# Kernel tuning notes

Hardware: AMD Instinct MI355X
Metric: run time of the kernel (lower is better)

The kernel has to match this reference:

```python
import jax, jax.numpy as jnp
import numpy as np

N_NODES = 100000
N_EDGES = 600000
F_IN, HID, CLS = 128, 128, 16


def sage_conv(x, src, dst, W_l, b_l, W_r, n_nodes):
    # mean aggregation of neighbor features: message x[src] scattered to dst
    msg = x[src]                                              # [E, F]
    agg = jax.ops.segment_sum(msg, dst, num_segments=n_nodes)  # [N, F]
    deg = jax.ops.segment_sum(jnp.ones((src.shape[0],), x.dtype), dst, num_segments=n_nodes)
    agg = agg / jnp.maximum(deg, 1.0)[:, None]
    # PyG SAGEConv: lin_l(agg) (with bias) + lin_r(x_root) (no bias)
    return agg @ W_l + b_l + x @ W_r


def setup_inputs() -> dict:
    key = jax.random.key(0)
    ks = jax.random.split(key, 6)
    x = jax.random.normal(ks[0], (N_NODES, F_IN), jnp.float32)
    edge_index = jax.random.randint(ks[1], (2, N_EDGES), 0, N_NODES, dtype=jnp.int64)
    s1 = 1.0 / np.sqrt(F_IN)
    s2 = 1.0 / np.sqrt(HID)
    return {
        "x": x,
        "edge_index": edge_index,
        "W1_l": jax.random.normal(ks[2], (F_IN, HID), jnp.float32) * s1,
        "b1": jnp.zeros((HID,), jnp.float32),
        "W1_r": jax.random.normal(ks[3], (F_IN, HID), jnp.float32) * s1,
        "W2_l": jax.random.normal(ks[4], (HID, CLS), jnp.float32) * s2,
        "b2": jnp.zeros((CLS,), jnp.float32),
        "W2_r": jax.random.normal(ks[5], (HID, CLS), jnp.float32) * s2,
    }


def reference(x, edge_index, W1_l, b1, W1_r, W2_l, b2, W2_r):
    n = x.shape[0]
    src, dst = edge_index[0], edge_index[1]
    h = sage_conv(x, src, dst, W1_l, b1, W1_r, n)
    h = jax.nn.relu(h)
    # F.dropout(training=self.training): identity in eval mode
    out = sage_conv(h, src, dst, W2_l, b2, W2_r, n)
    return jax.nn.log_softmax(out, axis=1)
```

## Files before the change

### kernel.cpp

```cpp
#include <hip/hip_runtime.h>
#include <cstdint>

#define N_NODES 100000
#define N_PAD 100096
#define N_EDGES 600000
#define F 128
#define CLS 16
#define CAP 64

typedef short bf16x8 __attribute__((ext_vector_type(8)));
typedef float f32x4 __attribute__((ext_vector_type(4)));

__device__ inline float bf2f(unsigned int lo16) { return __uint_as_float(lo16 << 16); }
__device__ inline unsigned short f2b(float f) {
    unsigned int u = __float_as_uint(f);
    return (unsigned short)((u + 0x7fffu + ((u >> 16) & 1u)) >> 16);
}

__global__ __launch_bounds__(256) void init_k(int* __restrict__ deg,
                                              const float* __restrict__ x,
                                              unsigned short* __restrict__ xb,
                                              const float* __restrict__ W1l,
                                              const float* __restrict__ W1r,
                                              const float* __restrict__ W2l,
                                              const float* __restrict__ W2r,
                                              unsigned short* __restrict__ w1t,
                                              unsigned short* __restrict__ w2t) {
    int b = blockIdx.x;
    if (b < 98) {
        int i = b * 1024 + threadIdx.x * 4;
#pragma unroll
        for (int k = 0; k < 4; k++)
            if (i + k < N_NODES) deg[i + k] = 0;
    } else if (b < 12598) {
        int i = (b - 98) * 256 + threadIdx.x;
        if (i < N_NODES * F / 4) {
            float4 v = ((const float4*)x)[i];
            ushort4 o;
            o.x = f2b(v.x); o.y = f2b(v.y); o.z = f2b(v.z); o.w = f2b(v.w);
            ((ushort4*)xb)[i] = o;
        }
    } else if (b < 12726) {
        int idx = (b - 12598) * 256 + threadIdx.x;
        int n = idx >> 8, k = idx & 255;
        float v = (k < F) ? W1l[k * F + n] : W1r[(k - F) * F + n];
        w1t[idx] = f2b(v);
    } else {
        int idx = (b - 12726) * 256 + threadIdx.x;
        if (idx < 32 * F) {
            int n = idx >> 7, k = idx & 127;
            float v = (n < CLS) ? W2l[k * CLS + n] : W2r[k * CLS + (n - CLS)];
            w2t[idx] = f2b(v);
        }
    }
}

__global__ void fill_k(const int* __restrict__ src, const int* __restrict__ dst,
                       int* __restrict__ deg, int* __restrict__ bucket) {
    int e = blockIdx.x * blockDim.x + threadIdx.x;
    if (e < N_EDGES) {
        int d = dst[e];
        int slot = atomicAdd(&deg[d], 1);
        if (slot < CAP) bucket[d * CAP + slot] = src[e];
    }
}

__global__ __launch_bounds__(256) void agg_b_k(const unsigned short* __restrict__ feat,
                                               const int* __restrict__ deg,
                                               const int* __restrict__ bucket,
                                               unsigned short* __restrict__ outagg) {
    int node = blockIdx.x * 4 + (threadIdx.x >> 6);
    int lane = threadIdx.x & 63;
    int r = lane >> 4;
    int f8 = (lane & 15) * 8;
    const int* bk = bucket + node * CAP;

    int d_raw = deg[node];
    int nb0r = bk[r];
    int nb1r = bk[4 + r];
    int nb0 = min(max(nb0r, 0), N_NODES - 1);
    int nb1 = min(max(nb1r, 0), N_NODES - 1);
    uint4 v0 = *(const uint4*)(feat + (size_t)nb0 * F + f8);
    uint4 v1 = *(const uint4*)(feat + (size_t)nb1 * F + f8);

    int d = min(d_raw, CAP);
    float acc[8] = {0.f, 0.f, 0.f, 0.f, 0.f, 0.f, 0.f, 0.f};
    if (r < d) {
        acc[0] += bf2f(v0.x & 0xffffu); acc[1] += bf2f(v0.x >> 16);
        acc[2] += bf2f(v0.y & 0xffffu); acc[3] += bf2f(v0.y >> 16);
        acc[4] += bf2f(v0.z & 0xffffu); acc[5] += bf2f(v0.z >> 16);
        acc[6] += bf2f(v0.w & 0xffffu); acc[7] += bf2f(v0.w >> 16);
    }
    if (4 + r < d) {
        acc[0] += bf2f(v1.x & 0xffffu); acc[1] += bf2f(v1.x >> 16);
        acc[2] += bf2f(v1.y & 0xffffu); acc[3] += bf2f(v1.y >> 16);
        acc[4] += bf2f(v1.z & 0xffffu); acc[5] += bf2f(v1.z >> 16);
        acc[6] += bf2f(v1.w & 0xffffu); acc[7] += bf2f(v1.w >> 16);
    }
    for (int j = 8; j < d; j += 8) {
        int i0 = j + r, i1 = j + 4 + r;
        bool ok0 = i0 < d, ok1 = i1 < d;
        int m0 = bk[ok0 ? i0 : 0];
        int m1 = bk[ok1 ? i1 : 0];
        uint4 w0 = *(const uint4*)(feat + (size_t)m0 * F + f8);
        uint4 w1 = *(const uint4*)(feat + (size_t)m1 * F + f8);
        if (ok0) {
            acc[0] += bf2f(w0.x & 0xffffu); acc[1] += bf2f(w0.x >> 16);
            acc[2] += bf2f(w0.y & 0xffffu); acc[3] += bf2f(w0.y >> 16);
            acc[4] += bf2f(w0.z & 0xffffu); acc[5] += bf2f(w0.z >> 16);
            acc[6] += bf2f(w0.w & 0xffffu); acc[7] += bf2f(w0.w >> 16);
        }
        if (ok1) {
            acc[0] += bf2f(w1.x & 0xffffu); acc[1] += bf2f(w1.x >> 16);
            acc[2] += bf2f(w1.y & 0xffffu); acc[3] += bf2f(w1.y >> 16);
            acc[4] += bf2f(w1.z & 0xffffu); acc[5] += bf2f(w1.z >> 16);
            acc[6] += bf2f(w1.w & 0xffffu); acc[7] += bf2f(w1.w >> 16);
        }
    }
#pragma unroll
    for (int i = 0; i < 8; i++) {
        acc[i] += __shfl_xor(acc[i], 16);
        acc[i] += __shfl_xor(acc[i], 32);
    }
    if (r == 0) {
        float inv = 1.0f / fmaxf((float)d, 1.0f);
        uint4 o;
        o.x = (unsigned int)f2b(acc[0] * inv) | ((unsigned int)f2b(acc[1] * inv) << 16);
        o.y = (unsigned int)f2b(acc[2] * inv) | ((unsigned int)f2b(acc[3] * inv) << 16);
        o.z = (unsigned int)f2b(acc[4] * inv) | ((unsigned int)f2b(acc[5] * inv) << 16);
        o.w = (unsigned int)f2b(acc[6] * inv) | ((unsigned int)f2b(acc[7] * inv) << 16);
        *(uint4*)(outagg + (size_t)node * F + f8) = o;
    }
}

__global__ __launch_bounds__(256) void gemm_fused(const unsigned short* __restrict__ Ab,
                                                  const unsigned short* __restrict__ Xb,
                                                  const unsigned short* __restrict__ Wt,
                                                  const float* __restrict__ bias,
                                                  const unsigned short* __restrict__ Wt2,
                                                  float* __restrict__ trL,
                                                  float* __restrict__ trR) {
    __shared__ unsigned short sw[64 * 512];
    __shared__ unsigned short sw2[8 * 512];
    int tid = threadIdx.x;
#pragma unroll
    for (int i = 0; i < 16; i++) {
        int idx8 = i * 256 + tid;
        uint4 v = ((const uint4*)Wt)[idx8];
        int n = idx8 >> 5;
        int k0 = (idx8 & 31) * 8;
        int ct = n >> 4, m = n & 15;
        int half = k0 >> 7, ks = (k0 >> 5) & 3, quad = (k0 >> 3) & 3;
        int frag = ct * 8 + ks * 2 + half;
        int lane = quad * 16 + m;
        *(uint4*)&sw[frag * 512 + lane * 8] = v;
    }
#pragma unroll
    for (int i = 0; i < 2; i++) {
        int idx8 = i * 256 + tid;
        uint4 v = ((const uint4*)Wt2)[idx8];
        int n = idx8 >> 4;
        int k0 = (idx8 & 15) * 8;
        int tile = n >> 4, m = n & 15;
        int ks = k0 >> 5, quad = (k0 >> 3) & 3;
        int frag = tile * 4 + ks;
        int lane = quad * 16 + m;
        *(uint4*)&sw2[frag * 512 + lane * 8] = v;
    }
    __syncthreads();

    int wave = tid >> 6, lane = tid & 63;
    int row0 = blockIdx.x * 128 + wave * 32;
    int m = lane & 15, quad = lane >> 4;
    int koff = quad * 8;

    const unsigned short* pa0 = Ab + (size_t)(row0 + m) * F + koff;
    const unsigned short* pa1 = pa0 + 16 * F;
    const unsigned short* px0 = Xb + (size_t)(row0 + m) * F + koff;
    const unsigned short* px1 = px0 + 16 * F;
    const unsigned short* swl = sw + lane * 8;

    f32x4 acc0[8], acc1[8];
#pragma unroll
    for (int ct = 0; ct < 8; ct++) { acc0[ct] = (f32x4){0,0,0,0}; acc1[ct] = (f32x4){0,0,0,0}; }

#pragma unroll
    for (int ks = 0; ks < 4; ks++) {
        bf16x8 a0 = *(const bf16x8*)(const void*)(pa0 + ks * 32);
        bf16x8 a1 = *(const bf16x8*)(const void*)(pa1 + ks * 32);
        bf16x8 x0 = *(const bf16x8*)(const void*)(px0 + ks * 32);
        bf16x8 x1 = *(const bf16x8*)(const void*)(px1 + ks * 32);
#pragma unroll
        for (int ct = 0; ct < 8; ct++) {
            bf16x8 bl = *(const bf16x8*)(const void*)(swl + (ct * 8 + ks * 2 + 0) * 512);
            bf16x8 br = *(const bf16x8*)(const void*)(swl + (ct * 8 + ks * 2 + 1) * 512);
            acc0[ct] = __builtin_amdgcn_mfma_f32_16x16x32_bf16(a0, bl, acc0[ct], 0, 0, 0);
            acc1[ct] = __builtin_amdgcn_mfma_f32_16x16x32_bf16(a1, bl, acc1[ct], 0, 0, 0);
            acc0[ct] = __builtin_amdgcn_mfma_f32_16x16x32_bf16(x0, br, acc0[ct], 0, 0, 0);
            acc1[ct] = __builtin_amdgcn_mfma_f32_16x16x32_bf16(x1, br, acc1[ct], 0, 0, 0);
        }
    }
    __syncthreads();

    int lr0 = wave * 32 + quad * 4;
#pragma unroll
    for (int ct = 0; ct < 8; ct++) {
        int n = ct * 16 + m;
        float bv = bias[n];
#pragma unroll
        for (int r = 0; r < 4; r++) {
            sw[(lr0 + r) * 132 + n]      = f2b(fmaxf(acc0[ct][r] + bv, 0.f));
            sw[(lr0 + 16 + r) * 132 + n] = f2b(fmaxf(acc1[ct][r] + bv, 0.f));
        }
    }
    __syncthreads();

    const unsigned short* hl0 = sw + (wave * 32 + m) * 132 + koff;
    const unsigned short* hl1 = sw + (wave * 32 + 16 + m) * 132 + koff;
    const unsigned short* sw2l = sw2 + lane * 8;

    f32x4 al0 = (f32x4){0,0,0,0}, al1 = (f32x4){0,0,0,0};
    f32x4 ar0 = (f32x4){0,0,0,0}, ar1 = (f32x4){0,0,0,0};
#pragma unroll
    for (int ks = 0; ks < 4; ks++) {
        bf16x8 h0 = *(const bf16x8*)(const void*)(hl0 + ks * 32);
        bf16x8 h1 = *(const bf16x8*)(const void*)(hl1 + ks * 32);
        bf16x8 wl = *(const bf16x8*)(const void*)(sw2l + (0 * 4 + ks) * 512);
        bf16x8 wr = *(const bf16x8*)(const void*)(sw2l + (1 * 4 + ks) * 512);
        al0 = __builtin_amdgcn_mfma_f32_16x16x32_bf16(h0, wl, al0, 0, 0, 0);
        al1 = __builtin_amdgcn_mfma_f32_16x16x32_bf16(h1, wl, al1, 0, 0, 0);
        ar0 = __builtin_amdgcn_mfma_f32_16x16x32_bf16(h0, wr, ar0, 0, 0, 0);
        ar1 = __builtin_amdgcn_mfma_f32_16x16x32_bf16(h1, wr, ar1, 0, 0, 0);
    }
    int r0 = row0 + quad * 4;
#pragma unroll
    for (int r = 0; r < 4; r++) {
        trL[(size_t)(r0 + r) * CLS + m]      = al0[r];
        trL[(size_t)(r0 + 16 + r) * CLS + m] = al1[r];
        trR[(size_t)(r0 + r) * CLS + m]      = ar0[r];
        trR[(size_t)(r0 + 16 + r) * CLS + m] = ar1[r];
    }
}

__global__ __launch_bounds__(256) void agg2sm_k(const float* __restrict__ trL,
                                                const float* __restrict__ trR,
                                                const int* __restrict__ deg,
                                                const int* __restrict__ bucket,
                                                const float* __restrict__ b2,
                                                float* __restrict__ out) {
    int node = blockIdx.x * 4 + (threadIdx.x >> 6);
    int lane = threadIdx.x & 63;
    int r = lane >> 2;
    int cq = (lane & 3) * 4;
    const int* bk = bucket + node * CAP;

    int d_raw = deg[node];
    int nbr = bk[r];
    int nb = min(max(nbr, 0), N_NODES - 1);
    float4 v = *(const float4*)(trL + (size_t)nb * CLS + cq);
    float4 selfR = *(const float4*)(trR + (size_t)node * CLS + cq);

    int d = min(d_raw, CAP);
    float4 acc = {0.f, 0.f, 0.f, 0.f};
    if (r < d) { acc.x += v.x; acc.y += v.y; acc.z += v.z; acc.w += v.w; }
    for (int j = 16; j < d; j += 16) {
        int idx = j + r;
        bool valid = idx < d;
        int m2 = bk[valid ? idx : 0];
        float4 w = *(const float4*)(trL + (size_t)m2 * CLS + cq);
        if (valid) { acc.x += w.x; acc.y += w.y; acc.z += w.z; acc.w += w.w; }
    }
#pragma unroll
    for (int off = 4; off <= 32; off <<= 1) {
        acc.x += __shfl_xor(acc.x, off);
        acc.y += __shfl_xor(acc.y, off);
        acc.z += __shfl_xor(acc.z, off);
        acc.w += __shfl_xor(acc.w, off);
    }
    float inv = 1.0f / fmaxf((float)d, 1.0f);
    float4 bb = *(const float4*)(b2 + cq);
    float vx = acc.x * inv + selfR.x + bb.x;
    float vy = acc.y * inv + selfR.y + bb.y;
    float vz = acc.z * inv + selfR.z + bb.z;
    float vw = acc.w * inv + selfR.w + bb.w;
    float mx = fmaxf(fmaxf(vx, vy), fmaxf(vz, vw));
    mx = fmaxf(mx, __shfl_xor(mx, 1));
    mx = fmaxf(mx, __shfl_xor(mx, 2));
    float sm = __expf(vx - mx) + __expf(vy - mx) + __expf(vz - mx) + __expf(vw - mx);
    sm += __shfl_xor(sm, 1);
    sm += __shfl_xor(sm, 2);
    float lg = __logf(sm);
    if (r == 0) {
        float4 o = {vx - mx - lg, vy - mx - lg, vz - mx - lg, vw - mx - lg};
        *(float4*)(out + (size_t)node * CLS + cq) = o;
    }
}


extern "C" void kernel_launch(void* const* d_in, const int* in_sizes, int n_in,
                              void* d_out, int out_size, void* d_ws, size_t ws_size,
                              hipStream_t stream) {
    const float* x   = (const float*)d_in[0];
    const int*   ei  = (const int*)d_in[1];
    const float* W1l = (const float*)d_in[2];
    const float* b1  = (const float*)d_in[3];
    const float* W1r = (const float*)d_in[4];
    const float* W2l = (const float*)d_in[5];
    const float* b2  = (const float*)d_in[6];
    const float* W2r = (const float*)d_in[7];
    float* out = (float*)d_out;

    const int* src = ei;
    const int* dst = ei + N_EDGES;

    char* ws = (char*)d_ws;
    size_t off = 0;
    auto alloc = [&](size_t bytes) { char* p = ws + off; off += (bytes + 127) / 128 * 128; return p; };
    int* deg    = (int*)alloc((size_t)N_NODES * 4);
    int* bucket = (int*)alloc((size_t)N_NODES * CAP * 4);
    unsigned short* xb   = (unsigned short*)alloc((size_t)N_PAD * F * 2);
    unsigned short* aggb = (unsigned short*)alloc((size_t)N_PAD * F * 2);
    float*          trL  = (float*)alloc((size_t)N_PAD * CLS * 4);
    float*          trR  = (float*)alloc((size_t)N_PAD * CLS * 4);
    unsigned short* w1t  = (unsigned short*)alloc((size_t)F * 256 * 2);
    unsigned short* w2t  = (unsigned short*)alloc((size_t)32 * F * 2);

    init_k<<<12743, 256, 0, stream>>>(deg, x, xb, W1l, W1r, W2l, W2r, w1t, w2t);
    fill_k<<<(N_EDGES + 255) / 256, 256, 0, stream>>>(src, dst, deg, bucket);
    agg_b_k<<<N_NODES / 4, 256, 0, stream>>>(xb, deg, bucket, aggb);
    gemm_fused<<<N_PAD / 128, 256, 0, stream>>>(aggb, xb, w1t, b1, w2t, trL, trR);
    agg2sm_k<<<N_NODES / 4, 256, 0, stream>>>(trL, trR, deg, bucket, b2, out);
}
```

Measured before the change: 225.1 us.

## Pre-swizzle weights into MFMA fragment order and read B operands from global

The init kernel now writes the transposed bf16 weights directly in MFMA fragment-major order. The fused GEMM therefore drops its per-block staging of the weights into shared memory and one barrier, and loads B fragments straight from global memory, where they are expected to stay cache resident. Shared memory shrinks to the hidden-activation buffer only, which may raise occupancy. The cost is that every B fragment load now goes to global/L2 with higher latency instead of LDS.

```diff
diff --git a/kernel.cpp b/kernel.cpp
--- a/kernel.cpp
+++ b/kernel.cpp
@@ -44,13 +44,17 @@
         int idx = (b - 12598) * 256 + threadIdx.x;
         int n = idx >> 8, k = idx & 255;
         float v = (k < F) ? W1l[k * F + n] : W1r[(k - F) * F + n];
-        w1t[idx] = f2b(v);
+        int ct = n >> 4, m = n & 15;
+        int half = k >> 7, ks = (k >> 5) & 3, quad = (k >> 3) & 3, j = k & 7;
+        w1t[(ct * 8 + ks * 2 + half) * 512 + (quad * 16 + m) * 8 + j] = f2b(v);
     } else {
         int idx = (b - 12726) * 256 + threadIdx.x;
         if (idx < 32 * F) {
             int n = idx >> 7, k = idx & 127;
             float v = (n < CLS) ? W2l[k * CLS + n] : W2r[k * CLS + (n - CLS)];
-            w2t[idx] = f2b(v);
+            int tile = n >> 4, m = n & 15;
+            int ks = (k >> 5) & 3, quad = (k >> 3) & 3, j = k & 7;
+            w2t[(tile * 4 + ks) * 512 + (quad * 16 + m) * 8 + j] = f2b(v);
         }
     }
 }
@@ -140,35 +144,8 @@
                                                   const unsigned short* __restrict__ Wt2,
                                                   float* __restrict__ trL,
                                                   float* __restrict__ trR) {
-    __shared__ unsigned short sw[64 * 512];
-    __shared__ unsigned short sw2[8 * 512];
+    __shared__ unsigned short sh[128 * 132];
     int tid = threadIdx.x;
-#pragma unroll
-    for (int i = 0; i < 16; i++) {
-        int idx8 = i * 256 + tid;
-        uint4 v = ((const uint4*)Wt)[idx8];
-        int n = idx8 >> 5;
-        int k0 = (idx8 & 31) * 8;
-        int ct = n >> 4, m = n & 15;
-        int half = k0 >> 7, ks = (k0 >> 5) & 3, quad = (k0 >> 3) & 3;
-        int frag = ct * 8 + ks * 2 + half;
-        int lane = quad * 16 + m;
-        *(uint4*)&sw[frag * 512 + lane * 8] = v;
-    }
-#pragma unroll
-    for (int i = 0; i < 2; i++) {
-        int idx8 = i * 256 + tid;
-        uint4 v = ((const uint4*)Wt2)[idx8];
-        int n = idx8 >> 4;
-        int k0 = (idx8 & 15) * 8;
-        int tile = n >> 4, m = n & 15;
-        int ks = k0 >> 5, quad = (k0 >> 3) & 3;
-        int frag = tile * 4 + ks;
-        int lane = quad * 16 + m;
-        *(uint4*)&sw2[frag * 512 + lane * 8] = v;
-    }
-    __syncthreads();
-
     int wave = tid >> 6, lane = tid & 63;
     int row0 = blockIdx.x * 128 + wave * 32;
     int m = lane & 15, quad = lane >> 4;
@@ -178,7 +155,7 @@
     const unsigned short* pa1 = pa0 + 16 * F;
     const unsigned short* px0 = Xb + (size_t)(row0 + m) * F + koff;
     const unsigned short* px1 = px0 + 16 * F;
-    const unsigned short* swl = sw + lane * 8;
+    const unsigned short* pw = Wt + lane * 8;
 
     f32x4 acc0[8], acc1[8];
 #pragma unroll
@@ -192,15 +169,14 @@
         bf16x8 x1 = *(const bf16x8*)(const void*)(px1 + ks * 32);
 #pragma unroll
         for (int ct = 0; ct < 8; ct++) {
-            bf16x8 bl = *(const bf16x8*)(const void*)(swl + (ct * 8 + ks * 2 + 0) * 512);
-            bf16x8 br = *(const bf16x8*)(const void*)(swl + (ct * 8 + ks * 2 + 1) * 512);
+            bf16x8 bl = *(const bf16x8*)(const void*)(pw + (ct * 8 + ks * 2 + 0) * 512);
+            bf16x8 br = *(const bf16x8*)(const void*)(pw + (ct * 8 + ks * 2 + 1) * 512);
             acc0[ct] = __builtin_amdgcn_mfma_f32_16x16x32_bf16(a0, bl, acc0[ct], 0, 0, 0);
             acc1[ct] = __builtin_amdgcn_mfma_f32_16x16x32_bf16(a1, bl, acc1[ct], 0, 0, 0);
             acc0[ct] = __builtin_amdgcn_mfma_f32_16x16x32_bf16(x0, br, acc0[ct], 0, 0, 0);
             acc1[ct] = __builtin_amdgcn_mfma_f32_16x16x32_bf16(x1, br, acc1[ct], 0, 0, 0);
         }
     }
-    __syncthreads();
 
     int lr0 = wave * 32 + quad * 4;
 #pragma unroll
@@ -209,15 +185,15 @@
         float bv = bias[n];
 #pragma unroll
         for (int r = 0; r < 4; r++) {
-            sw[(lr0 + r) * 132 + n]      = f2b(fmaxf(acc0[ct][r] + bv, 0.f));
-            sw[(lr0 + 16 + r) * 132 + n] = f2b(fmaxf(acc1[ct][r] + bv, 0.f));
+            sh[(lr0 + r) * 132 + n]      = f2b(fmaxf(acc0[ct][r] + bv, 0.f));
+            sh[(lr0 + 16 + r) * 132 + n] = f2b(fmaxf(acc1[ct][r] + bv, 0.f));
         }
     }
     __syncthreads();
 
-    const unsigned short* hl0 = sw + (wave * 32 + m) * 132 + koff;
-    const unsigned short* hl1 = sw + (wave * 32 + 16 + m) * 132 + koff;
-    const unsigned short* sw2l = sw2 + lane * 8;
+    const unsigned short* hl0 = sh + (wave * 32 + m) * 132 + koff;
+    const unsigned short* hl1 = sh + (wave * 32 + 16 + m) * 132 + koff;
+    const unsigned short* pw2 = Wt2 + lane * 8;
 
     f32x4 al0 = (f32x4){0,0,0,0}, al1 = (f32x4){0,0,0,0};
     f32x4 ar0 = (f32x4){0,0,0,0}, ar1 = (f32x4){0,0,0,0};
@@ -225,8 +201,8 @@
     for (int ks = 0; ks < 4; ks++) {
         bf16x8 h0 = *(const bf16x8*)(const void*)(hl0 + ks * 32);
         bf16x8 h1 = *(const bf16x8*)(const void*)(hl1 + ks * 32);
-        bf16x8 wl = *(const bf16x8*)(const void*)(sw2l + (0 * 4 + ks) * 512);
-        bf16x8 wr = *(const bf16x8*)(const void*)(sw2l + (1 * 4 + ks) * 512);
+        bf16x8 wl = *(const bf16x8*)(const void*)(pw2 + (0 * 4 + ks) * 512);
+        bf16x8 wr = *(const bf16x8*)(const void*)(pw2 + (1 * 4 + ks) * 512);
         al0 = __builtin_amdgcn_mfma_f32_16x16x32_bf16(h0, wl, al0, 0, 0, 0);
         al1 = __builtin_amdgcn_mfma_f32_16x16x32_bf16(h1, wl, al1, 0, 0, 0);
         ar0 = __builtin_amdgcn_mfma_f32_16x16x32_bf16(h0, wr, ar0, 0, 0, 0);
```

Measured after the change: 225.4 us. No clear change (+0.1%).
